# Performance work log

Hardware: AMD Instinct MI355X
Metric: run time of the kernel (lower is better)

Reference implementation:

```python
import jax, jax.numpy as jnp
import numpy as np

N_WIDTH = 8
N_ORDER = 2
N_ELEMENTS = 1024
N_NODES = N_ELEMENTS * N_ORDER + 1  # 2049
N_SAMPLES = 4096
X_MIN = 0.0
X_MAX = 1.0


def _ref_nodes():
    return np.linspace(-1.0, 1.0, N_ORDER + 1)


def _lagrange(x):
    # x: [I, K] -> [I, K, P]
    nodes = _ref_nodes()
    cols = []
    for j in range(N_ORDER + 1):
        p = jnp.ones_like(x)
        for m in range(N_ORDER + 1):
            if j != m:
                p = p * (x - nodes[m]) / (nodes[j] - nodes[m])
        cols.append(p)
    return jnp.stack(cols, axis=-1)


def _dlagrange(x):
    nodes = _ref_nodes()
    cols = []
    for j in range(N_ORDER + 1):
        y = jnp.zeros_like(x)
        for i in range(N_ORDER + 1):
            if i != j:
                k = jnp.ones_like(x) / (nodes[j] - nodes[i])
                for m in range(N_ORDER + 1):
                    if m != i and m != j:
                        k = k * (x - nodes[m]) / (nodes[j] - nodes[m])
                y = y + k
        cols.append(y)
    return jnp.stack(cols, axis=-1)


def _ddlagrange(x):
    nodes = _ref_nodes()
    cols = []
    for j in range(N_ORDER + 1):
        y = jnp.zeros_like(x)
        for i in range(N_ORDER + 1):
            if i != j:
                k_sum = jnp.zeros_like(x)
                for m in range(N_ORDER + 1):
                    if m != i and m != j:
                        k_prod = jnp.ones_like(x) / (nodes[j] - nodes[m])
                        for n in range(N_ORDER + 1):
                            if n != i and n != j and n != m:
                                k_prod = k_prod * (x - nodes[n]) / (nodes[j] - nodes[n])
                        k_sum = k_sum + k_prod
                y = y + (1.0 / (nodes[j] - nodes[i])) * k_sum
        cols.append(y)
    return jnp.stack(cols, axis=-1)


def setup_inputs() -> dict:
    key = jax.random.key(0)
    k1, k2 = jax.random.split(key)
    x = jax.random.uniform(k1, (N_SAMPLES,), dtype=jnp.float32)  # in [x_min, x_max)
    weight = jax.random.normal(k2, (N_WIDTH, N_NODES), dtype=jnp.float32) * 0.02
    return {"x": x, "weight": weight}


def reference(x, weight):
    # replicate 1-D input across width: [I] -> [I, K]
    x2 = jnp.repeat(x[:, None], N_WIDTH, axis=-1)
    x_shift = (N_NODES - 1) * (x2 - X_MIN) / (X_MAX - X_MIN)
    id_el = jnp.clip(jnp.floor(x_shift / N_ORDER), 0, N_ELEMENTS - 1)
    nodes_l = (id_el * N_ORDER).astype(jnp.int32)  # [I, K]
    nodes_lf = jax.lax.stop_gradient(nodes_l.astype(x_shift.dtype))
    # reference coord: (x_shift - 0.5*(l + r)) / (0.5*(r - l)) with r = l + n_order
    x_t = (x_shift - (nodes_lf + 0.5 * N_ORDER)) / (0.5 * N_ORDER)

    delta_x = 0.5 * N_ORDER * (X_MAX - X_MIN) / (N_NODES - 1)
    phi_loc = _lagrange(x_t)                       # [I, K, P]
    dphi_loc = _dlagrange(x_t) / delta_x
    ddphi_loc = _ddlagrange(x_t) / (delta_x * delta_x)

    I, K = x2.shape
    P = N_ORDER + 1
    idx = nodes_l[:, :, None] + jnp.arange(P)      # [I, K, P] global node ids
    ii = jnp.arange(I)[:, None, None]
    kk = jnp.arange(K)[None, :, None]
    phi_ikp = jnp.zeros((I, K, N_NODES), x2.dtype).at[ii, kk, idx].set(phi_loc)
    dphi_ikp = jnp.zeros((I, K, N_NODES), x2.dtype).at[ii, kk, idx].set(dphi_loc)
    ddphi_ikp = jnp.zeros((I, K, N_NODES), x2.dtype).at[ii, kk, idx].set(ddphi_loc)

    t_ik = jnp.einsum('kp,ikp->ik', weight, phi_ikp)
    dt_ik = jnp.einsum('kp,ikp->ik', weight, dphi_ikp)
    ddt_ik = jnp.einsum('kp,ikp->ik', weight, ddphi_ikp)
    return (t_ik, dt_ik, ddt_ik, phi_ikp, dphi_ikp, ddphi_ikp)
```

## Files before the change

### kernel.cpp

```cpp
#include <hip/hip_runtime.h>


#define KN_NODES    2049
#define KN_SAMPLES  4096
#define KN_IK       (KN_SAMPLES * 8)
#define KN_HEAD     (3 * KN_IK)
#define KN_PHI_LEN  ((size_t)KN_IK * KN_NODES)
#define KN_ROWF     (8 * KN_NODES)
#define KN_NF4      (KN_ROWF / 4)

__global__ __launch_bounds__(256)
void KANN_all(const float* __restrict__ x, const float* __restrict__ w,
              float* __restrict__ out) {
    const int i = blockIdx.x;
    const int y = blockIdx.y;

    float xv  = x[i];
    float xs  = 2048.0f * xv;
    float fid = floorf(0.5f * xs);
    fid = fminf(fmaxf(fid, 0.0f), 1023.0f);
    int   nl  = 2 * (int)fid;
    float x_t = xs - (float)nl - 1.0f;

    float b0, b1, b2;
    if (y == 0)      { b0 = 0.5f * x_t * (x_t - 1.0f); b1 = 1.0f - x_t * x_t; b2 = 0.5f * x_t * (x_t + 1.0f); }
    else if (y == 1) { b0 = (x_t - 0.5f) * 2048.0f; b1 = -4096.0f * x_t; b2 = (x_t + 0.5f) * 2048.0f; }
    else             { b0 = 4194304.0f; b1 = -8388608.0f; b2 = 4194304.0f; }

    if (y == 0 && threadIdx.x < 8) {
        int k = threadIdx.x;
        const float* wk = w + k * KN_NODES + nl;
        float w0 = wk[0], w1 = wk[1], w2 = wk[2];
        float p0 = 0.5f * x_t * (x_t - 1.0f);
        float p1 = 1.0f - x_t * x_t;
        float p2 = 0.5f * x_t * (x_t + 1.0f);
        int ik = i * 8 + k;
        out[ik]             = w0 * p0 + w1 * p1 + w2 * p2;
        out[KN_IK + ik]     = (w0 * (x_t - 0.5f) - 2.0f * w1 * x_t + w2 * (x_t + 0.5f)) * 2048.0f;
        out[2 * KN_IK + ik] = (w0 - 2.0f * w1 + w2) * 4194304.0f;
    }

    float* base = out + KN_HEAD + (size_t)y * KN_PHI_LEN + (size_t)i * KN_ROWF;
    const float4 zero4 = make_float4(0.0f, 0.0f, 0.0f, 0.0f);

    for (int f = threadIdx.x; f < KN_NF4; f += 256) {
        int e0 = f << 2;
        int r  = e0 >> 11;
        int c  = (e0 & 2047) - r;
        if (c < 0) { r -= 1; c += KN_NODES; }
        int  d0   = c - nl;
        bool hot  = (d0 >= -3 && d0 <= 2) || (c >= 2046 && nl <= 2);
        if (__builtin_expect(__any(hot), 0)) {
            float vv[4];
#pragma unroll
            for (int j = 0; j < 4; ++j) {
                int cj = c + j;
                if (cj > 2048) cj -= KN_NODES;
                int d = cj - nl;
                vv[j] = (d == 0) ? b0 : ((d == 1) ? b1 : ((d == 2) ? b2 : 0.0f));
            }
            *reinterpret_cast<float4*>(base + e0) = make_float4(vv[0], vv[1], vv[2], vv[3]);
        } else {
            *reinterpret_cast<float4*>(base + e0) = zero4;
        }
    }
}

extern "C" void kernel_launch(void* const* d_in, const int* in_sizes, int n_in,
                              void* d_out, int out_size, void* d_ws, size_t ws_size,
                              hipStream_t stream) {
    const float* x = (const float*)d_in[0];
    const float* w = (const float*)d_in[1];
    float* out = (float*)d_out;
    KANN_all<<<dim3(KN_SAMPLES, 3), dim3(256), 0, stream>>>(x, w, out);
}
```

Measured before the change: 168.8 us.

## Replace fused dense fill with memset plus sparse scatter kernel

Zero-fills the whole output with an async memset, then launches a flat kernel that computes the weighted sums and scatters only the three nonzero basis values per row. This removes the per-element hot/cold test and index arithmetic from the dense write loop. In exchange it adds a second pass over the output region via the memset plus a scatter kernel with uncoalesced writes and an extra launch.

```diff
diff --git a/kernel.cpp b/kernel.cpp
--- a/kernel.cpp
+++ b/kernel.cpp
@@ -6,63 +6,45 @@
 #define KN_IK       (KN_SAMPLES * 8)
 #define KN_HEAD     (3 * KN_IK)
 #define KN_PHI_LEN  ((size_t)KN_IK * KN_NODES)
-#define KN_ROWF     (8 * KN_NODES)
-#define KN_NF4      (KN_ROWF / 4)
 
-__global__ __launch_bounds__(256)
-void KANN_all(const float* __restrict__ x, const float* __restrict__ w,
-              float* __restrict__ out) {
-    const int i = blockIdx.x;
-    const int y = blockIdx.y;
-
-    float xv  = x[i];
+__device__ __forceinline__ void kann_coord(float xv, int& nl, float& x_t) {
     float xs  = 2048.0f * xv;
     float fid = floorf(0.5f * xs);
     fid = fminf(fmaxf(fid, 0.0f), 1023.0f);
-    int   nl  = 2 * (int)fid;
-    float x_t = xs - (float)nl - 1.0f;
+    nl  = 2 * (int)fid;
+    x_t = xs - (float)nl - 1.0f;
+}
 
-    float b0, b1, b2;
-    if (y == 0)      { b0 = 0.5f * x_t * (x_t - 1.0f); b1 = 1.0f - x_t * x_t; b2 = 0.5f * x_t * (x_t + 1.0f); }
-    else if (y == 1) { b0 = (x_t - 0.5f) * 2048.0f; b1 = -4096.0f * x_t; b2 = (x_t + 0.5f) * 2048.0f; }
-    else             { b0 = 4194304.0f; b1 = -8388608.0f; b2 = 4194304.0f; }
+__global__ __launch_bounds__(256)
+void KANN_scatter(const float* __restrict__ x, const float* __restrict__ w,
+                  float* __restrict__ out) {
+    int t = blockIdx.x * 256 + threadIdx.x;
 
-    if (y == 0 && threadIdx.x < 8) {
-        int k = threadIdx.x;
+    if (t < KN_IK) {
+        int ik = t;
+        int i = ik >> 3, k = ik & 7;
+        int nl; float x_t; kann_coord(x[i], nl, x_t);
         const float* wk = w + k * KN_NODES + nl;
         float w0 = wk[0], w1 = wk[1], w2 = wk[2];
         float p0 = 0.5f * x_t * (x_t - 1.0f);
         float p1 = 1.0f - x_t * x_t;
         float p2 = 0.5f * x_t * (x_t + 1.0f);
-        int ik = i * 8 + k;
         out[ik]             = w0 * p0 + w1 * p1 + w2 * p2;
         out[KN_IK + ik]     = (w0 * (x_t - 0.5f) - 2.0f * w1 * x_t + w2 * (x_t + 0.5f)) * 2048.0f;
         out[2 * KN_IK + ik] = (w0 - 2.0f * w1 + w2) * 4194304.0f;
-    }
-
-    float* base = out + KN_HEAD + (size_t)y * KN_PHI_LEN + (size_t)i * KN_ROWF;
-    const float4 zero4 = make_float4(0.0f, 0.0f, 0.0f, 0.0f);
-
-    for (int f = threadIdx.x; f < KN_NF4; f += 256) {
-        int e0 = f << 2;
-        int r  = e0 >> 11;
-        int c  = (e0 & 2047) - r;
-        if (c < 0) { r -= 1; c += KN_NODES; }
-        int  d0   = c - nl;
-        bool hot  = (d0 >= -3 && d0 <= 2) || (c >= 2046 && nl <= 2);
-        if (__builtin_expect(__any(hot), 0)) {
-            float vv[4];
-#pragma unroll
-            for (int j = 0; j < 4; ++j) {
-                int cj = c + j;
-                if (cj > 2048) cj -= KN_NODES;
-                int d = cj - nl;
-                vv[j] = (d == 0) ? b0 : ((d == 1) ? b1 : ((d == 2) ? b2 : 0.0f));
-            }
-            *reinterpret_cast<float4*>(base + e0) = make_float4(vv[0], vv[1], vv[2], vv[3]);
-        } else {
-            *reinterpret_cast<float4*>(base + e0) = zero4;
-        }
+    } else {
+        int s = t - KN_IK;
+        if (s >= 3 * KN_IK) return;
+        int y  = s >> 15;
+        int ik = s & (KN_IK - 1);
+        int i  = ik >> 3;
+        int nl; float x_t; kann_coord(x[i], nl, x_t);
+        float b0, b1, b2;
+        if (y == 0)      { b0 = 0.5f * x_t * (x_t - 1.0f); b1 = 1.0f - x_t * x_t; b2 = 0.5f * x_t * (x_t + 1.0f); }
+        else if (y == 1) { b0 = (x_t - 0.5f) * 2048.0f; b1 = -4096.0f * x_t; b2 = (x_t + 0.5f) * 2048.0f; }
+        else             { b0 = 4194304.0f; b1 = -8388608.0f; b2 = 4194304.0f; }
+        float* p = out + KN_HEAD + (size_t)y * KN_PHI_LEN + (size_t)ik * KN_NODES + nl;
+        p[0] = b0; p[1] = b1; p[2] = b2;
     }
 }
 
@@ -72,5 +54,9 @@
     const float* x = (const float*)d_in[0];
     const float* w = (const float*)d_in[1];
     float* out = (float*)d_out;
-    KANN_all<<<dim3(KN_SAMPLES, 3), dim3(256), 0, stream>>>(x, w, out);
+
+    hipMemsetAsync(out, 0, (size_t)out_size * sizeof(float), stream);
+
+    const int total = 4 * KN_IK;
+    KANN_scatter<<<dim3(total / 256), dim3(256), 0, stream>>>(x, w, out);
 }
```

Result: faster. 151.7 us (-10.1%).
